# Kernel tuning notes

Measured on AMD Instinct MI355X. Metric: run time of the kernel, lower is better.

The kernel has to match this reference:

```python
import jax, jax.numpy as jnp
import numpy as np

H = 20  # hidden_size

def _lstm_layer(x_tbf, w_ih, w_hh, b_ih, b_hh):
    # x_tbf: [T, B, F]; torch gate order: i, f, g, o
    T, B, _ = x_tbf.shape
    # precompute input projections once: [T, B, 4H]
    xproj = jnp.einsum('tbf,gf->tbg', x_tbf, w_ih) + b_ih + b_hh

    def step(carry, xp_t):
        h, c = carry
        gates = xp_t + h @ w_hh.T  # [B, 4H]
        i, f, g, o = jnp.split(gates, 4, axis=-1)
        i = jax.nn.sigmoid(i)
        f = jax.nn.sigmoid(f)
        g = jnp.tanh(g)
        o = jax.nn.sigmoid(o)
        c = f * c + i * g
        h = o * jnp.tanh(c)
        return (h, c), h

    h0 = jnp.zeros((B, H), dtype=x_tbf.dtype)
    c0 = jnp.zeros((B, H), dtype=x_tbf.dtype)
    (_, _), hs = jax.lax.scan(step, (h0, c0), xproj)
    return hs  # [T, B, H]

def setup_inputs() -> dict:
    key = jax.random.key(0)
    ks = jax.random.split(key, 11)
    F_in = 10
    s_ih0 = 1.0 / np.sqrt(H)
    inp = {
        'x': jax.random.normal(ks[0], (4096, 512, F_in), dtype=jnp.float32),
        'w_ih0': jax.random.uniform(ks[1], (4 * H, F_in), minval=-s_ih0, maxval=s_ih0),
        'w_hh0': jax.random.uniform(ks[2], (4 * H, H), minval=-s_ih0, maxval=s_ih0),
        'b_ih0': jax.random.uniform(ks[3], (4 * H,), minval=-s_ih0, maxval=s_ih0),
        'b_hh0': jax.random.uniform(ks[4], (4 * H,), minval=-s_ih0, maxval=s_ih0),
        'w_ih1': jax.random.uniform(ks[5], (4 * H, H), minval=-s_ih0, maxval=s_ih0),
        'w_hh1': jax.random.uniform(ks[6], (4 * H, H), minval=-s_ih0, maxval=s_ih0),
        'b_ih1': jax.random.uniform(ks[7], (4 * H,), minval=-s_ih0, maxval=s_ih0),
        'b_hh1': jax.random.uniform(ks[8], (4 * H,), minval=-s_ih0, maxval=s_ih0),
        'w_fc': jax.random.uniform(ks[9], (1, H), minval=-s_ih0, maxval=s_ih0),
        'b_fc': jax.random.uniform(ks[10], (1,), minval=-s_ih0, maxval=s_ih0),
    }
    return inp

def reference(x, w_ih0, w_hh0, b_ih0, b_hh0, w_ih1, w_hh1, b_ih1, b_hh1, w_fc, b_fc):
    # x: [B, T, F] (batch_first) -> [T, B, F] for scan
    x_tbf = jnp.swapaxes(x, 0, 1)
    h1 = _lstm_layer(x_tbf, w_ih0, w_hh0, b_ih0, b_hh0)  # [T, B, H]
    h2 = _lstm_layer(h1, w_ih1, w_hh1, b_ih1, b_hh1)     # [T, B, H]
    last = h2[-1]                                          # [B, H]
    return last @ w_fc.T + b_fc                            # [B, 1]
```

## Files before the change

kernel.cpp:

```cpp
#include <hip/hip_runtime.h>

#define T_STEPS 512
#define HS 20
#define F0 10
#define BPB 6
#define NB_TOT 4096
#define NBLK ((NB_TOT + BPB - 1) / BPB)
#define CHK 16
#define NCH (T_STEPS / CHK)
#define XCHW (CHK * BPB * F0)

__device__ __forceinline__ float sigmoid_fast(float v) {
    return __fdividef(1.f, 1.f + __expf(-v));
}
__device__ __forceinline__ float tanh_fast(float v) {
    return 1.f - __fdividef(2.f, __expf(2.f * v) + 1.f);
}
#define PIN(v) asm volatile("" : "+v"(v))

__device__ __forceinline__ float stage_ld(const float* __restrict__ x,
                                          int bx, int cc, int i) {
    const int s = i / (BPB * F0);
    const int r = i - s * (BPB * F0);
    const int b = r / F0;
    const int f = r - b * F0;
    int gb = bx * BPB + b; gb = (gb < NB_TOT) ? gb : (NB_TOT - 1);
    int ts = cc * CHK + s; ts = (ts < T_STEPS) ? ts : (T_STEPS - 1);
    return x[(size_t)gb * (T_STEPS * F0) + ts * F0 + f];
}

__global__ __launch_bounds__(256, 3)
void lstm2_fc_kernel(const float* __restrict__ x,
                     const float* __restrict__ wih0, const float* __restrict__ whh0,
                     const float* __restrict__ bih0, const float* __restrict__ bhh0,
                     const float* __restrict__ wih1, const float* __restrict__ whh1,
                     const float* __restrict__ bih1, const float* __restrict__ bhh1,
                     const float* __restrict__ wfc,  const float* __restrict__ bfc,
                     float* __restrict__ out)
{
    const int tid   = threadIdx.x;
    const int wid   = tid >> 6;
    const int lane  = tid & 63;
    const int g     = (lane / HS) % 3;
    const int u     = lane % HS;
    const int layer = wid >> 1;
    const int half  = wid & 1;
    const int q0    = 2 * half;
    const int bx    = blockIdx.x;
    const int bgA   = bx * BPB + g;
    const int bgBr  = bx * BPB + g + 3;
    const bool okB  = (bgBr < NB_TOT);

    __shared__ float s_h0[2][BPB][HS];
    __shared__ float s_h1[2][BPB][HS];
    __shared__ float ex0[2][BPB][HS][4];
    __shared__ float ex1[2][BPB][HS][4];
    __shared__ float xs[2][XCHW];

    const int i3c = (tid + 768 < XCHW) ? (tid + 768) : (XCHW - 1);
    float sv0 = stage_ld(x, bx, 0, tid);
    float sv1 = stage_ld(x, bx, 0, tid + 256);
    float sv2 = stage_ld(x, bx, 0, tid + 512);
    float sv3 = stage_ld(x, bx, 0, i3c);

    for (int i = tid; i < 2 * BPB * HS; i += 256) {
        (&s_h0[0][0][0])[i] = 0.f;
        (&s_h1[0][0][0])[i] = 0.f;
    }

    float w[2][2 * HS], bias[2];
    if (layer == 0) {
        #pragma unroll
        for (int qh = 0; qh < 2; ++qh) {
            const int row = (q0 + qh) * HS + u;
            #pragma unroll
            for (int f = 0; f < F0; ++f) { w[qh][f] = wih0[row * F0 + f]; PIN(w[qh][f]); }
            #pragma unroll
            for (int j = 0; j < HS; ++j) { w[qh][F0 + j] = whh0[row * HS + j]; PIN(w[qh][F0 + j]); }
            bias[qh] = bih0[row] + bhh0[row]; PIN(bias[qh]);
        }
    } else {
        #pragma unroll
        for (int qh = 0; qh < 2; ++qh) {
            const int row = (q0 + qh) * HS + u;
            #pragma unroll
            for (int j = 0; j < HS; ++j) { w[qh][j]      = wih1[row * HS + j]; PIN(w[qh][j]); }
            #pragma unroll
            for (int j = 0; j < HS; ++j) { w[qh][HS + j] = whh1[row * HS + j]; PIN(w[qh][HS + j]); }
            bias[qh] = bih1[row] + bhh1[row]; PIN(bias[qh]);
        }
    }

    float cA = 0.f, cB = 0.f;

    xs[0][tid]       = sv0;
    xs[0][tid + 256] = sv1;
    xs[0][tid + 512] = sv2;
    xs[0][i3c]       = sv3;
    __syncthreads();

    #pragma unroll 1
    for (int t = 0; t < T_STEPS + 3; ++t) {
        const bool do_stage = ((t & (CHK - 1)) == 0) && (((t >> 4) + 1) < NCH);
        const int scc = (t >> 4) + 1;
        float tv0, tv1, tv2, tv3;
        if (do_stage) {
            tv0 = stage_ld(x, bx, scc, tid);
            tv1 = stage_ld(x, bx, scc, tid + 256);
            tv2 = stage_ld(x, bx, scc, tid + 512);
            tv3 = stage_ld(x, bx, scc, i3c);
        }

        if (layer == 0) {
            if (t >= 1 && t <= T_STEPS) {
                const int sl = (t - 1) & 1;
                const float4 eA = *(const float4*)&ex0[sl][g][u][0];
                const float4 eB = *(const float4*)&ex0[sl][g + 3][u][0];
                cA = fmaf(eA.y, cA, eA.x * eA.z);
                cB = fmaf(eB.y, cB, eB.x * eB.z);
                s_h0[sl][g][u]     = eA.w * tanh_fast(cA);
                s_h0[sl][g + 3][u] = eB.w * tanh_fast(cB);
            }
            if (t < T_STEPS) {
                float a0A = bias[0], a1A = bias[1];
                float a0B = bias[0], a1B = bias[1];
                const float* xr = &xs[(t >> 4) & 1][(t & (CHK - 1)) * (BPB * F0)];
                const float2* xpA = (const float2*)(xr + g * F0);
                const float2* xpB = (const float2*)(xr + (g + 3) * F0);
                #pragma unroll
                for (int f2 = 0; f2 < F0 / 2; ++f2) {
                    const int f = 2 * f2;
                    const float2 vA = xpA[f2], vB = xpB[f2];
                    a0A = fmaf(vA.x, w[0][f], a0A); a0A = fmaf(vA.y, w[0][f + 1], a0A);
                    a1A = fmaf(vA.x, w[1][f], a1A); a1A = fmaf(vA.y, w[1][f + 1], a1A);
                    a0B = fmaf(vB.x, w[0][f], a0B); a0B = fmaf(vB.y, w[0][f + 1], a0B);
                    a1B = fmaf(vB.x, w[1][f], a1B); a1B = fmaf(vB.y, w[1][f + 1], a1B);
                }
                const float* hpA = &s_h0[(t + 1) & 1][g][0];
                const float* hpB = &s_h0[(t + 1) & 1][g + 3][0];
                #pragma unroll
                for (int q4 = 0; q4 < HS / 4; ++q4) {
                    const float4 hA = *(const float4*)(hpA + 4 * q4);
                    const float4 hB = *(const float4*)(hpB + 4 * q4);
                    const float eA[4] = {hA.x, hA.y, hA.z, hA.w};
                    const float eB[4] = {hB.x, hB.y, hB.z, hB.w};
                    #pragma unroll
                    for (int e = 0; e < 4; ++e) {
                        const int k = F0 + 4 * q4 + e;
                        a0A = fmaf(eA[e], w[0][k], a0A);  a0B = fmaf(eB[e], w[0][k], a0B);
                        a1A = fmaf(eA[e], w[1][k], a1A);  a1B = fmaf(eB[e], w[1][k], a1B);
                    }
                }
                float act0A, act1A, act0B, act1B;
                if (half == 0) {
                    act0A = sigmoid_fast(a0A); act1A = sigmoid_fast(a1A);
                    act0B = sigmoid_fast(a0B); act1B = sigmoid_fast(a1B);
                } else {
                    act0A = tanh_fast(a0A);    act1A = sigmoid_fast(a1A);
                    act0B = tanh_fast(a0B);    act1B = sigmoid_fast(a1B);
                }
                *(float2*)&ex0[t & 1][g][u][q0]     = make_float2(act0A, act1A);
                *(float2*)&ex0[t & 1][g + 3][u][q0] = make_float2(act0B, act1B);
            }
        } else {
            if (t >= 3) {
                const int sl = (t - 3) & 1;
                const float4 eA = *(const float4*)&ex1[sl][g][u][0];
                const float4 eB = *(const float4*)&ex1[sl][g + 3][u][0];
                cA = fmaf(eA.y, cA, eA.x * eA.z);
                cB = fmaf(eB.y, cB, eB.x * eB.z);
                s_h1[sl][g][u]     = eA.w * tanh_fast(cA);
                s_h1[sl][g + 3][u] = eB.w * tanh_fast(cB);
            }
            if (t >= 2 && t < T_STEPS + 2) {
                float a0A = bias[0], a1A = bias[1];
                float a0B = bias[0], a1B = bias[1];
                const float* hpA = &s_h0[t & 1][g][0];
                const float* hpB = &s_h0[t & 1][g + 3][0];
                #pragma unroll
                for (int q4 = 0; q4 < HS / 4; ++q4) {
                    const float4 hA = *(const float4*)(hpA + 4 * q4);
                    const float4 hB = *(const float4*)(hpB + 4 * q4);
                    const float eA[4] = {hA.x, hA.y, hA.z, hA.w};
                    const float eB[4] = {hB.x, hB.y, hB.z, hB.w};
                    #pragma unroll
                    for (int e = 0; e < 4; ++e) {
                        const int k = 4 * q4 + e;
                        a0A = fmaf(eA[e], w[0][k], a0A);  a0B = fmaf(eB[e], w[0][k], a0B);
                        a1A = fmaf(eA[e], w[1][k], a1A);  a1B = fmaf(eB[e], w[1][k], a1B);
                    }
                }
                const float* ppA = &s_h1[(t + 1) & 1][g][0];
                const float* ppB = &s_h1[(t + 1) & 1][g + 3][0];
                #pragma unroll
                for (int q4 = 0; q4 < HS / 4; ++q4) {
                    const float4 hA = *(const float4*)(ppA + 4 * q4);
                    const float4 hB = *(const float4*)(ppB + 4 * q4);
                    const float eA[4] = {hA.x, hA.y, hA.z, hA.w};
                    const float eB[4] = {hB.x, hB.y, hB.z, hB.w};
                    #pragma unroll
                    for (int e = 0; e < 4; ++e) {
                        const int k = HS + 4 * q4 + e;
                        a0A = fmaf(eA[e], w[0][k], a0A);  a0B = fmaf(eB[e], w[0][k], a0B);
                        a1A = fmaf(eA[e], w[1][k], a1A);  a1B = fmaf(eB[e], w[1][k], a1B);
                    }
                }
                float act0A, act1A, act0B, act1B;
                if (half == 0) {
                    act0A = sigmoid_fast(a0A); act1A = sigmoid_fast(a1A);
                    act0B = sigmoid_fast(a0B); act1B = sigmoid_fast(a1B);
                } else {
                    act0A = tanh_fast(a0A);    act1A = sigmoid_fast(a1A);
                    act0B = tanh_fast(a0B);    act1B = sigmoid_fast(a1B);
                }
                *(float2*)&ex1[t & 1][g][u][q0]     = make_float2(act0A, act1A);
                *(float2*)&ex1[t & 1][g + 3][u][q0] = make_float2(act0B, act1B);
            }
        }

        if (do_stage) {
            float* xw = &xs[scc & 1][0];
            xw[tid]       = tv0;
            xw[tid + 256] = tv1;
            xw[tid + 512] = tv2;
            xw[i3c]       = tv3;
        }
        __syncthreads();
    }

    if (wid == 3 && lane < 60 && u == 0) {
        const int sl = (T_STEPS - 1) & 1;
        float oA = bfc[0], oB = bfc[0];
        #pragma unroll
        for (int j = 0; j < HS; ++j) {
            oA = fmaf(s_h1[sl][g][j],     wfc[j], oA);
            oB = fmaf(s_h1[sl][g + 3][j], wfc[j], oB);
        }
        out[bgA] = oA;
        if (okB) out[bgBr] = oB;
    }
}

extern "C" void kernel_launch(void* const* d_in, const int* in_sizes, int n_in,
                              void* d_out, int out_size, void* d_ws, size_t ws_size,
                              hipStream_t stream) {
    const float* x    = (const float*)d_in[0];
    const float* wih0 = (const float*)d_in[1];
    const float* whh0 = (const float*)d_in[2];
    const float* bih0 = (const float*)d_in[3];
    const float* bhh0 = (const float*)d_in[4];
    const float* wih1 = (const float*)d_in[5];
    const float* whh1 = (const float*)d_in[6];
    const float* bih1 = (const float*)d_in[7];
    const float* bhh1 = (const float*)d_in[8];
    const float* wfc  = (const float*)d_in[9];
    const float* bfc  = (const float*)d_in[10];
    float* out = (float*)d_out;

    dim3 grid(NBLK), block(256);
    hipLaunchKernelGGL(lstm2_fc_kernel, grid, block, 0, stream,
                       x, wih0, whh0, bih0, bhh0,
                       wih1, whh1, bih1, bhh1, wfc, bfc, out);
}
```

Measured before the change: 849.8 us.

## Finalize LSTM cell state in a second barrier phase, shortening pipeline latency

```diff
diff --git a/kernel.cpp b/kernel.cpp
--- a/kernel.cpp
+++ b/kernel.cpp
@@ -46,6 +46,7 @@
     const int layer = wid >> 1;
     const int half  = wid & 1;
     const int q0    = 2 * half;
+    const int gfin  = (half == 0) ? g : (g + 3);
     const int bx    = blockIdx.x;
     const int bgA   = bx * BPB + g;
     const int bgBr  = bx * BPB + g + 3;
@@ -53,15 +54,15 @@
 
     __shared__ float s_h0[2][BPB][HS];
     __shared__ float s_h1[2][BPB][HS];
-    __shared__ float ex0[2][BPB][HS][4];
-    __shared__ float ex1[2][BPB][HS][4];
+    __shared__ float ex0[BPB][HS][4];
+    __shared__ float ex1[BPB][HS][4];
     __shared__ float xs[2][XCHW];
 
-    const int i3c = (tid + 768 < XCHW) ? (tid + 768) : (XCHW - 1);
+    const bool st3 = (tid < XCHW - 768);
     float sv0 = stage_ld(x, bx, 0, tid);
     float sv1 = stage_ld(x, bx, 0, tid + 256);
     float sv2 = stage_ld(x, bx, 0, tid + 512);
-    float sv3 = stage_ld(x, bx, 0, i3c);
+    float sv3 = st3 ? stage_ld(x, bx, 0, tid + 768) : 0.f;
 
     for (int i = tid; i < 2 * BPB * HS; i += 256) {
         (&s_h0[0][0][0])[i] = 0.f;
@@ -91,16 +92,16 @@
         }
     }
 
-    float cA = 0.f, cB = 0.f;
+    float cc = 0.f;
 
     xs[0][tid]       = sv0;
     xs[0][tid + 256] = sv1;
     xs[0][tid + 512] = sv2;
-    xs[0][i3c]       = sv3;
+    if (st3) xs[0][tid + 768] = sv3;
     __syncthreads();
 
     #pragma unroll 1
-    for (int t = 0; t < T_STEPS + 3; ++t) {
+    for (int t = 0; t <= T_STEPS; ++t) {
         const bool do_stage = ((t & (CHK - 1)) == 0) && (((t >> 4) + 1) < NCH);
         const int scc = (t >> 4) + 1;
         float tv0, tv1, tv2, tv3;
@@ -108,22 +109,14 @@
             tv0 = stage_ld(x, bx, scc, tid);
             tv1 = stage_ld(x, bx, scc, tid + 256);
             tv2 = stage_ld(x, bx, scc, tid + 512);
-            tv3 = stage_ld(x, bx, scc, i3c);
+            tv3 = st3 ? stage_ld(x, bx, scc, tid + 768) : 0.f;
         }
 
         if (layer == 0) {
-            if (t >= 1 && t <= T_STEPS) {
-                const int sl = (t - 1) & 1;
-                const float4 eA = *(const float4*)&ex0[sl][g][u][0];
-                const float4 eB = *(const float4*)&ex0[sl][g + 3][u][0];
-                cA = fmaf(eA.y, cA, eA.x * eA.z);
-                cB = fmaf(eB.y, cB, eB.x * eB.z);
-                s_h0[sl][g][u]     = eA.w * tanh_fast(cA);
-                s_h0[sl][g + 3][u] = eB.w * tanh_fast(cB);
-            }
             if (t < T_STEPS) {
-                float a0A = bias[0], a1A = bias[1];
-                float a0B = bias[0], a1B = bias[1];
+                float xa0A = bias[0], xa1A = bias[1];
+                float xa0B = bias[0], xa1B = bias[1];
+                float ha0A = 0.f, ha1A = 0.f, ha0B = 0.f, ha1B = 0.f;
                 const float* xr = &xs[(t >> 4) & 1][(t & (CHK - 1)) * (BPB * F0)];
                 const float2* xpA = (const float2*)(xr + g * F0);
                 const float2* xpB = (const float2*)(xr + (g + 3) * F0);
@@ -131,10 +124,10 @@
                 for (int f2 = 0; f2 < F0 / 2; ++f2) {
                     const int f = 2 * f2;
                     const float2 vA = xpA[f2], vB = xpB[f2];
-                    a0A = fmaf(vA.x, w[0][f], a0A); a0A = fmaf(vA.y, w[0][f + 1], a0A);
-                    a1A = fmaf(vA.x, w[1][f], a1A); a1A = fmaf(vA.y, w[1][f + 1], a1A);
-                    a0B = fmaf(vB.x, w[0][f], a0B); a0B = fmaf(vB.y, w[0][f + 1], a0B);
-                    a1B = fmaf(vB.x, w[1][f], a1B); a1B = fmaf(vB.y, w[1][f + 1], a1B);
+                    xa0A = fmaf(vA.x, w[0][f], xa0A); xa0A = fmaf(vA.y, w[0][f + 1], xa0A);
+                    xa1A = fmaf(vA.x, w[1][f], xa1A); xa1A = fmaf(vA.y, w[1][f + 1], xa1A);
+                    xa0B = fmaf(vB.x, w[0][f], xa0B); xa0B = fmaf(vB.y, w[0][f + 1], xa0B);
+                    xa1B = fmaf(vB.x, w[1][f], xa1B); xa1B = fmaf(vB.y, w[1][f + 1], xa1B);
                 }
                 const float* hpA = &s_h0[(t + 1) & 1][g][0];
                 const float* hpB = &s_h0[(t + 1) & 1][g + 3][0];
@@ -147,10 +140,12 @@
                     #pragma unroll
                     for (int e = 0; e < 4; ++e) {
                         const int k = F0 + 4 * q4 + e;
-                        a0A = fmaf(eA[e], w[0][k], a0A);  a0B = fmaf(eB[e], w[0][k], a0B);
-                        a1A = fmaf(eA[e], w[1][k], a1A);  a1B = fmaf(eB[e], w[1][k], a1B);
+                        ha0A = fmaf(eA[e], w[0][k], ha0A);  ha0B = fmaf(eB[e], w[0][k], ha0B);
+                        ha1A = fmaf(eA[e], w[1][k], ha1A);  ha1B = fmaf(eB[e], w[1][k], ha1B);
                     }
                 }
+                const float a0A = xa0A + ha0A, a1A = xa1A + ha1A;
+                const float a0B = xa0B + ha0B, a1B = xa1B + ha1B;
                 float act0A, act1A, act0B, act1B;
                 if (half == 0) {
                     act0A = sigmoid_fast(a0A); act1A = sigmoid_fast(a1A);
@@ -159,24 +154,16 @@
                     act0A = tanh_fast(a0A);    act1A = sigmoid_fast(a1A);
                     act0B = tanh_fast(a0B);    act1B = sigmoid_fast(a1B);
                 }
-                *(float2*)&ex0[t & 1][g][u][q0]     = make_float2(act0A, act1A);
-                *(float2*)&ex0[t & 1][g + 3][u][q0] = make_float2(act0B, act1B);
+                *(float2*)&ex0[g][u][q0]     = make_float2(act0A, act1A);
+                *(float2*)&ex0[g + 3][u][q0] = make_float2(act0B, act1B);
             }
         } else {
-            if (t >= 3) {
-                const int sl = (t - 3) & 1;
-                const float4 eA = *(const float4*)&ex1[sl][g][u][0];
-                const float4 eB = *(const float4*)&ex1[sl][g + 3][u][0];
-                cA = fmaf(eA.y, cA, eA.x * eA.z);
-                cB = fmaf(eB.y, cB, eB.x * eB.z);
-                s_h1[sl][g][u]     = eA.w * tanh_fast(cA);
-                s_h1[sl][g + 3][u] = eB.w * tanh_fast(cB);
-            }
-            if (t >= 2 && t < T_STEPS + 2) {
-                float a0A = bias[0], a1A = bias[1];
-                float a0B = bias[0], a1B = bias[1];
-                const float* hpA = &s_h0[t & 1][g][0];
-                const float* hpB = &s_h0[t & 1][g + 3][0];
+            if (t >= 1) {
+                float xa0A = bias[0], xa1A = bias[1];
+                float xa0B = bias[0], xa1B = bias[1];
+                float ha0A = 0.f, ha1A = 0.f, ha0B = 0.f, ha1B = 0.f;
+                const float* hpA = &s_h0[(t - 1) & 1][g][0];
+                const float* hpB = &s_h0[(t - 1) & 1][g + 3][0];
                 #pragma unroll
                 for (int q4 = 0; q4 < HS / 4; ++q4) {
                     const float4 hA = *(const float4*)(hpA + 4 * q4);
@@ -186,12 +173,12 @@
                     #pragma unroll
                     for (int e = 0; e < 4; ++e) {
                         const int k = 4 * q4 + e;
-                        a0A = fmaf(eA[e], w[0][k], a0A);  a0B = fmaf(eB[e], w[0][k], a0B);
-                        a1A = fmaf(eA[e], w[1][k], a1A);  a1B = fmaf(eB[e], w[1][k], a1B);
+                        xa0A = fmaf(eA[e], w[0][k], xa0A);  xa0B = fmaf(eB[e], w[0][k], xa0B);
+                        xa1A = fmaf(eA[e], w[1][k], xa1A);  xa1B = fmaf(eB[e], w[1][k], xa1B);
                     }
                 }
-                const float* ppA = &s_h1[(t + 1) & 1][g][0];
-                const float* ppB = &s_h1[(t + 1) & 1][g + 3][0];
+                const float* ppA = &s_h1[t & 1][g][0];
+                const float* ppB = &s_h1[t & 1][g + 3][0];
                 #pragma unroll
                 for (int q4 = 0; q4 < HS / 4; ++q4) {
                     const float4 hA = *(const float4*)(ppA + 4 * q4);
@@ -201,10 +188,12 @@
                     #pragma unroll
                     for (int e = 0; e < 4; ++e) {
                         const int k = HS + 4 * q4 + e;
-                        a0A = fmaf(eA[e], w[0][k], a0A);  a0B = fmaf(eB[e], w[0][k], a0B);
-                        a1A = fmaf(eA[e], w[1][k], a1A);  a1B = fmaf(eB[e], w[1][k], a1B);
+                        ha0A = fmaf(eA[e], w[0][k], ha0A);  ha0B = fmaf(eB[e], w[0][k], ha0B);
+                        ha1A = fmaf(eA[e], w[1][k], ha1A);  ha1B = fmaf(eB[e], w[1][k], ha1B);
                     }
                 }
+                const float a0A = xa0A + ha0A, a1A = xa1A + ha1A;
+                const float a0B = xa0B + ha0B, a1B = xa1B + ha1B;
                 float act0A, act1A, act0B, act1B;
                 if (half == 0) {
                     act0A = sigmoid_fast(a0A); act1A = sigmoid_fast(a1A);
@@ -213,8 +202,8 @@
                     act0A = tanh_fast(a0A);    act1A = sigmoid_fast(a1A);
                     act0B = tanh_fast(a0B);    act1B = sigmoid_fast(a1B);
                 }
-                *(float2*)&ex1[t & 1][g][u][q0]     = make_float2(act0A, act1A);
-                *(float2*)&ex1[t & 1][g + 3][u][q0] = make_float2(act0B, act1B);
+                *(float2*)&ex1[g][u][q0]     = make_float2(act0A, act1A);
+                *(float2*)&ex1[g + 3][u][q0] = make_float2(act0B, act1B);
             }
         }
 
@@ -223,7 +212,22 @@
             xw[tid]       = tv0;
             xw[tid + 256] = tv1;
             xw[tid + 512] = tv2;
-            xw[i3c]       = tv3;
+            if (st3) xw[tid + 768] = tv3;
+        }
+        __syncthreads();
+
+        if (layer == 0) {
+            if (t < T_STEPS) {
+                const float4 e = *(const float4*)&ex0[gfin][u][0];
+                cc = fmaf(e.y, cc, e.x * e.z);
+                s_h0[t & 1][gfin][u] = e.w * tanh_fast(cc);
+            }
+        } else {
+            if (t >= 1) {
+                const float4 e = *(const float4*)&ex1[gfin][u][0];
+                cc = fmaf(e.y, cc, e.x * e.z);
+                s_h1[(t - 1) & 1][gfin][u] = e.w * tanh_fast(cc);
+            }
         }
         __syncthreads();
     }
```

Measured after the change: 780.7 us. 1.09x faster.
